# Optimization experiments

Measured on AMD Instinct MI355X. Metric: run time of the kernel, lower is better.

The kernel has to match this reference:

```python
import jax, jax.numpy as jnp
import numpy as np

N = 100000
E = 1600000
EPS = 1e-5


def _layer_norm(x, g, b):
    mu = jnp.mean(x, axis=-1, keepdims=True)
    var = jnp.mean((x - mu) ** 2, axis=-1, keepdims=True)
    return (x - mu) * jax.lax.rsqrt(var + EPS) * g + b


def _sage(x, src, dst, wl, bl, wr):
    # mean aggregation of neighbor messages x[src] into dst, then linear
    msg_sum = jax.ops.segment_sum(x[src], dst, num_segments=N)          # [N, d_in]
    cnt = jax.ops.segment_sum(jnp.ones((src.shape[0],), x.dtype), dst, num_segments=N)
    mean = msg_sum / jnp.maximum(cnt, 1.0)[:, None]
    return mean @ wl.T + bl + x @ wr.T  # lin_l(mean) + lin_r(x), bias only on lin_l


def setup_inputs() -> dict:
    key = jax.random.key(0)
    ks = jax.random.split(key, 16)
    dims = [(9, 64), (64, 128), (128, 128), (128, 128)]
    inp = {
        "x": jax.random.normal(ks[0], (N, 9), dtype=jnp.float32),
        "edge_index": jax.random.randint(ks[1], (2, E), 0, N, dtype=jnp.int32),
    }
    for i, (din, dout) in enumerate(dims, start=1):
        s = 1.0 / np.sqrt(din)
        inp[f"w{i}l"] = jax.random.uniform(ks[2 + 3 * i], (dout, din), jnp.float32, -s, s)
        inp[f"b{i}"] = jnp.zeros((dout,), jnp.float32)
        inp[f"w{i}r"] = jax.random.uniform(ks[3 + 3 * i], (dout, din), jnp.float32, -s, s)
        inp[f"g{i}"] = jnp.ones((dout,), jnp.float32)
        inp[f"be{i}"] = jnp.zeros((dout,), jnp.float32)
    return inp


def reference(x, edge_index,
              w1l, b1, w1r, g1, be1,
              w2l, b2, w2r, g2, be2,
              w3l, b3, w3r, g3, be3,
              w4l, b4, w4r, g4, be4):
    src, dst = edge_index[0], edge_index[1]
    h = jax.nn.relu(_layer_norm(_sage(x, src, dst, w1l, b1, w1r), g1, be1))
    h = jax.nn.relu(_layer_norm(_sage(h, src, dst, w2l, b2, w2r), g2, be2))
    h = jax.nn.relu(_layer_norm(_sage(h, src, dst, w3l, b3, w3r), g3, be3))
    h = _layer_norm(_sage(h, src, dst, w4l, b4, w4r), g4, be4)
    return h
```

## Files before the change

kernel.cpp:

```cpp
#include <hip/hip_runtime.h>
#include <hip/hip_bf16.h>
#include <math.h>

#define N_NODES 100000
#define EPS 1e-5f
#define B2SH 11
#define NPB2 2048
#define NBUCK2 ((N_NODES + NPB2 - 1) / NPB2)
#define NPART 256

typedef __attribute__((ext_vector_type(8))) short bf16x8;
typedef __attribute__((ext_vector_type(4))) float f32x4;

__device__ __forceinline__ float bflo(unsigned int u) { return __uint_as_float(u << 16); }
__device__ __forceinline__ float bfhi(unsigned int u) { return __uint_as_float(u & 0xffff0000u); }
__device__ __forceinline__ unsigned short fbits(float f) {
    __hip_bfloat16 h = __float2bfloat16(f);
    return *reinterpret_cast<unsigned short*>(&h);
}
__device__ __forceinline__ void stv(float* p, float y) { *p = y; }
__device__ __forceinline__ void stv(__hip_bfloat16* p, float y) { *p = __float2bfloat16(y); }
__device__ __forceinline__ unsigned char f8enc(float y) {
    return (unsigned char)((unsigned int)__builtin_amdgcn_cvt_pk_fp8_f32(y, y, 0, false) & 0xffu);
}

__global__ void part_hist(const int* __restrict__ dst, int E, int* __restrict__ blkhist) {
    __shared__ int h[NBUCK2];
    int b = blockIdx.x;
    int slice = (E + NPART - 1) / NPART;
    int s0 = b * slice;
    int s1 = min(E, s0 + slice);
    for (int i = threadIdx.x; i < NBUCK2; i += 256) h[i] = 0;
    __syncthreads();
    for (int e = s0 + threadIdx.x; e < s1; e += 256) atomicAdd(&h[dst[e] >> B2SH], 1);
    __syncthreads();
    for (int i = threadIdx.x; i < NBUCK2; i += 256) blkhist[i * NPART + b] = h[i];
}

__global__ void part_offsets(const int* __restrict__ blkhist, int* __restrict__ blkoffs,
                             int* __restrict__ bbase2, int* __restrict__ row_ptr, int E) {
    __shared__ int tot[NBUCK2];
    __shared__ int sbase[NBUCK2 + 1];
    int j = threadIdx.x;
    if (j < NBUCK2) {
        int run = 0;
#pragma unroll 8
        for (int b = 0; b < NPART; ++b) {
            blkoffs[j * NPART + b] = run;
            run += blkhist[j * NPART + b];
        }
        tot[j] = run;
    }
    __syncthreads();
    if (j == 0) {
        int run = 0;
        for (int i = 0; i < NBUCK2; ++i) {
            sbase[i] = run;
            run += tot[i];
        }
        sbase[NBUCK2] = run;
        row_ptr[N_NODES] = E;
    }
    __syncthreads();
    if (j <= NBUCK2) bbase2[j] = sbase[j];
    if (j < NBUCK2) {
        int base = sbase[j];
#pragma unroll 8
        for (int b = 0; b < NPART; ++b) blkoffs[j * NPART + b] += base;
    }
}

__global__ void part_scatter(const int* __restrict__ src, const int* __restrict__ dst, int E,
                             const int* __restrict__ blkoffs, unsigned int* __restrict__ pairs) {
    __shared__ int pos[NBUCK2];
    int b = blockIdx.x;
    int slice = (E + NPART - 1) / NPART;
    int s0 = b * slice;
    int s1 = min(E, s0 + slice);
    for (int i = threadIdx.x; i < NBUCK2; i += 256) pos[i] = blkoffs[i * NPART + b];
    __syncthreads();
    for (int e = s0 + threadIdx.x; e < s1; e += 256) {
        int d = dst[e];
        int jb = d >> B2SH;
        int p = atomicAdd(&pos[jb], 1);
        pairs[p] = ((unsigned int)src[e] << B2SH) | (unsigned int)(d & (NPB2 - 1));
    }
}

__global__ __launch_bounds__(1024) void bucket_build2(const unsigned int* __restrict__ pairs,
                                                      const int* __restrict__ bbase2,
                                                      int* __restrict__ row_ptr,
                                                      int* __restrict__ col) {
    __shared__ int lcnt[NPB2];
    __shared__ int lofs[NPB2];
    __shared__ int part[1024];
    int bk = blockIdx.x;
    int base = bbase2[bk];
    int cntb = bbase2[bk + 1] - base;
    int node0 = bk << B2SH;
    int t = threadIdx.x;
    lcnt[t] = 0;
    lcnt[t + 1024] = 0;
    __syncthreads();
    for (int i = t; i < cntb; i += 1024) atomicAdd(&lcnt[pairs[base + i] & (NPB2 - 1)], 1);
    __syncthreads();
    int a0 = lcnt[2 * t], a1 = lcnt[2 * t + 1];
    part[t] = a0 + a1;
    __syncthreads();
    for (int off = 1; off < 1024; off <<= 1) {
        int v = (t >= off) ? part[t - off] : 0;
        __syncthreads();
        part[t] += v;
        __syncthreads();
    }
    int excl = part[t] - (a0 + a1);
    lofs[2 * t] = excl;
    lofs[2 * t + 1] = excl + a0;
    __syncthreads();
#pragma unroll
    for (int k = 0; k < 2; ++k) {
        int ln = 2 * t + k;
        int node = node0 + ln;
        if (node < N_NODES) row_ptr[node] = base + lofs[ln];
    }
    lcnt[t] = 0;
    lcnt[t + 1024] = 0;
    __syncthreads();
    for (int i = t; i < cntb; i += 1024) {
        unsigned int v = pairs[base + i];
        int ld = v & (NPB2 - 1);
        int s = v >> B2SH;
        int p = base + lofs[ld] + atomicAdd(&lcnt[ld], 1);
        col[p] = s;
    }
}

__global__ void agg9_kernel(const float* __restrict__ x, const int* __restrict__ row_ptr,
                            const int* __restrict__ col, float* __restrict__ mean, int n) {
    int node = (blockIdx.x * blockDim.x + threadIdx.x) >> 6;
    int lane = threadIdx.x & 63;
    int wv = threadIdx.x >> 6;
    __shared__ float red[4][64];
    float acc = 0.f;
    int start = 0, end = 0;
    if (node < n) {
        start = row_ptr[node];
        end = row_ptr[node + 1];
        int g = lane / 9;
        int f = lane - g * 9;
        if (g < 7 && end > start) {
            for (int p = start + g; p < end; p += 28) {
#pragma unroll
                for (int i = 0; i < 4; ++i) {
                    int q = p + i * 7;
                    int idx = (q < end) ? q : end - 1;
                    float v = x[(size_t)col[idx] * 9 + f];
                    if (q >= end) v = 0.f;
                    acc += v;
                }
            }
        }
    }
    red[wv][lane] = acc;
    __syncthreads();
    if (node < n && lane < 9) {
        float s = red[wv][lane];
#pragma unroll
        for (int k = 1; k < 7; ++k) s += red[wv][lane + 9 * k];
        float inv = 1.f / fmaxf((float)(end - start), 1.f);
        mean[(size_t)node * 9 + lane] = s * inv;
    }
}

__global__ void agg64_kernel(const unsigned char* __restrict__ h8, const int* __restrict__ row_ptr,
                             const int* __restrict__ col, unsigned short* __restrict__ mean, int n) {
    int node = (blockIdx.x * blockDim.x + threadIdx.x) >> 6;
    int lane = threadIdx.x & 63;
    if (node >= n) return;
    int start = row_ptr[node], end = row_ptr[node + 1];
    int deg = end - start;
    if (deg <= 0) {
        mean[(size_t)node * 64 + lane] = 0;
        return;
    }
    const unsigned char* hl = h8 + lane;
    float acc = 0.f;
    int p = start;
    int nfull = start + (deg & ~7);
    for (; p < nfull; p += 8) {
#pragma unroll
        for (int i = 0; i < 8; ++i) {
            unsigned int off = (unsigned int)col[p + i] << 6;
            unsigned int u = (unsigned int)hl[off];
            acc += __builtin_amdgcn_cvt_f32_fp8(u, 0);
        }
    }
    if (p < end) {
#pragma unroll
        for (int i = 0; i < 8; ++i) {
            int q = p + i;
            int idx = (q < end) ? q : p;
            unsigned int off = (unsigned int)col[idx] << 6;
            unsigned int u = (unsigned int)hl[off];
            float v = __builtin_amdgcn_cvt_f32_fp8(u, 0);
            if (q < end) acc += v;
        }
    }
    mean[(size_t)node * 64 + lane] = fbits(acc / (float)deg);
}

__global__ void agg128_kernel(const unsigned char* __restrict__ h8, const int* __restrict__ row_ptr,
                              const int* __restrict__ col, unsigned short* __restrict__ mean, int n) {
    int node = (blockIdx.x * blockDim.x + threadIdx.x) >> 6;
    int lane = threadIdx.x & 63;
    if (node >= n) return;
    int start = row_ptr[node], end = row_ptr[node + 1];
    int deg = end - start;
    if (deg <= 0) {
        *(unsigned int*)&mean[(size_t)node * 128 + lane * 2] = 0u;
        return;
    }
    const unsigned char* hl = h8 + lane * 2;
    float ax = 0.f, ay = 0.f;
    int p = start;
    int nfull = start + (deg & ~7);
    for (; p < nfull; p += 8) {
#pragma unroll
        for (int i = 0; i < 8; ++i) {
            unsigned int off = (unsigned int)col[p + i] << 7;
            unsigned int u = (unsigned int)*(const unsigned short*)(hl + off);
            ax += __builtin_amdgcn_cvt_f32_fp8(u, 0);
            ay += __builtin_amdgcn_cvt_f32_fp8(u, 1);
        }
    }
    if (p < end) {
#pragma unroll
        for (int i = 0; i < 8; ++i) {
            int q = p + i;
            int idx = (q < end) ? q : p;
            unsigned int off = (unsigned int)col[idx] << 7;
            unsigned int u = (unsigned int)*(const unsigned short*)(hl + off);
            float v0 = __builtin_amdgcn_cvt_f32_fp8(u, 0);
            float v1 = __builtin_amdgcn_cvt_f32_fp8(u, 1);
            if (q < end) {
                ax += v0;
                ay += v1;
            }
        }
    }
    float inv = 1.f / (float)deg;
    unsigned int lo = fbits(ax * inv);
    unsigned int hi = fbits(ay * inv);
    *(unsigned int*)&mean[(size_t)node * 128 + lane * 2] = lo | (hi << 16);
}

__global__ void wtrans_kernel(const float* __restrict__ wl, const float* __restrict__ wr,
                              int din, int dout, float* __restrict__ wt) {
    int i = blockIdx.x * blockDim.x + threadIdx.x;
    int K2 = 2 * din;
    if (i >= K2 * dout) return;
    int k = i / dout, j = i % dout;
    wt[k * dout + j] = (k < din) ? wl[j * din + k] : wr[j * din + (k - din)];
}

__global__ void packw_kernel(const float* __restrict__ wl, const float* __restrict__ wr,
                             int din, unsigned short* __restrict__ bpack) {
    int K2 = 2 * din;
    int total = K2 * 128;
    int i = blockIdx.x * 256 + threadIdx.x;
    if (i >= total) return;
    int e = i & 7;
    int lane = (i >> 3) & 63;
    int rest = i >> 9;
    int KSTEPS = din / 16;
    int t = rest / KSTEPS, ks = rest % KSTEPS;
    int j = t * 16 + (lane & 15);
    int k = ks * 32 + (lane >> 4) * 8 + e;
    float w = (k < din) ? wl[j * din + k] : wr[j * din + (k - din)];
    bpack[i] = fbits(w);
}

template <int DIN, int DOUT, bool RELU, typename OT>
__global__ __launch_bounds__(256) void linear_ln_kernel(
    const float* __restrict__ meanp, const float* __restrict__ hp,
    const float* __restrict__ wt, const float* __restrict__ bias,
    const float* __restrict__ g, const float* __restrict__ be,
    OT* __restrict__ out, unsigned char* __restrict__ out8, int n) {
    constexpr int K2 = 2 * DIN;
    constexpr int NCOL = DOUT / 4;
    constexpr int NROW = 256 / NCOL;
    constexpr int TN = 4 * NROW;
    constexpr int ASTR = TN + 4;
    constexpr int OSTR = DOUT + 4;
    constexpr int SMEMF = (K2 * ASTR > TN * OSTR) ? K2 * ASTR : TN * OSTR;
    __shared__ float smem[SMEMF];

    int tid = threadIdx.x;
    int n0base = blockIdx.x * TN;

    for (int idx = tid; idx < TN * K2; idx += 256) {
        int nn = idx / K2;
        int k = idx % K2;
        int node = n0base + nn;
        float v = 0.f;
        if (node < n)
            v = (k < DIN) ? meanp[(size_t)node * DIN + k] : hp[(size_t)node * DIN + (k - DIN)];
        smem[k * ASTR + nn] = v;
    }
    __syncthreads();

    int colt = tid % NCOL;
    int rowt = tid / NCOL;
    int j0 = colt * 4;
    int nn0 = rowt * 4;

    float acc[4][4];
#pragma unroll
    for (int i = 0; i < 4; ++i)
#pragma unroll
        for (int j = 0; j < 4; ++j) acc[i][j] = 0.f;

#pragma unroll 2
    for (int k = 0; k < K2; ++k) {
        float4 a = *(const float4*)&smem[k * ASTR + nn0];
        float4 w = *(const float4*)&wt[k * DOUT + j0];
        acc[0][0] = fmaf(a.x, w.x, acc[0][0]);
        acc[0][1] = fmaf(a.x, w.y, acc[0][1]);
        acc[0][2] = fmaf(a.x, w.z, acc[0][2]);
        acc[0][3] = fmaf(a.x, w.w, acc[0][3]);
        acc[1][0] = fmaf(a.y, w.x, acc[1][0]);
        acc[1][1] = fmaf(a.y, w.y, acc[1][1]);
        acc[1][2] = fmaf(a.y, w.z, acc[1][2]);
        acc[1][3] = fmaf(a.y, w.w, acc[1][3]);
        acc[2][0] = fmaf(a.z, w.x, acc[2][0]);
        acc[2][1] = fmaf(a.z, w.y, acc[2][1]);
        acc[2][2] = fmaf(a.z, w.z, acc[2][2]);
        acc[2][3] = fmaf(a.z, w.w, acc[2][3]);
        acc[3][0] = fmaf(a.w, w.x, acc[3][0]);
        acc[3][1] = fmaf(a.w, w.y, acc[3][1]);
        acc[3][2] = fmaf(a.w, w.z, acc[3][2]);
        acc[3][3] = fmaf(a.w, w.w, acc[3][3]);
    }
    __syncthreads();

    float4 bj = *(const float4*)&bias[j0];
#pragma unroll
    for (int i = 0; i < 4; ++i) {
        float4 o;
        o.x = acc[i][0] + bj.x;
        o.y = acc[i][1] + bj.y;
        o.z = acc[i][2] + bj.z;
        o.w = acc[i][3] + bj.w;
        *(float4*)&smem[(nn0 + i) * OSTR + j0] = o;
    }
    __syncthreads();

    int wid = tid >> 6, lane = tid & 63;
    for (int nn = wid; nn < TN; nn += 4) {
        int node = n0base + nn;
        if (node >= n) continue;
        float v0 = smem[nn * OSTR + lane];
        float v1 = (DOUT == 128) ? smem[nn * OSTR + 64 + lane] : 0.f;
        float s = v0 + v1;
        float ss = v0 * v0 + v1 * v1;
#pragma unroll
        for (int off = 32; off > 0; off >>= 1) {
            s += __shfl_xor(s, off);
            ss += __shfl_xor(ss, off);
        }
        float mu = s / DOUT;
        float var = ss / DOUT - mu * mu;
        float inv = rsqrtf(var + EPS);
        float y0 = (v0 - mu) * inv * g[lane] + be[lane];
        if (RELU) y0 = fmaxf(y0, 0.f);
        stv(&out[(size_t)node * DOUT + lane], y0);
        if (out8) out8[(size_t)node * DOUT + lane] = f8enc(y0);
        if (DOUT == 128) {
            float y1 = (v1 - mu) * inv * g[64 + lane] + be[64 + lane];
            if (RELU) y1 = fmaxf(y1, 0.f);
            stv(&out[(size_t)node * DOUT + 64 + lane], y1);
            if (out8) out8[(size_t)node * DOUT + 64 + lane] = f8enc(y1);
        }
    }
}

template <int DIN, bool RELU, typename OT>
__global__ __launch_bounds__(256) void mfma_linear_ln(
    const unsigned short* __restrict__ meanb, const unsigned short* __restrict__ hb,
    const unsigned short* __restrict__ bpack, const float* __restrict__ bias,
    const float* __restrict__ g, const float* __restrict__ be, OT* __restrict__ out,
    unsigned char* __restrict__ out8, int n) {
    constexpr int KSTEPS = DIN / 16;
    int tid = threadIdx.x;
    int w = tid >> 6, l = tid & 63;
    int n0 = blockIdx.x * 64 + w * 16;
    int arow = l & 15;
    int koff = (l >> 4) * 8;
    int anode = n0 + arow;
    if (anode >= n) anode = n - 1;
    const unsigned short* mrow = meanb + (size_t)anode * DIN;
    const unsigned short* hrow = hb + (size_t)anode * DIN;

    f32x4 acc[8];
#pragma unroll
    for (int t = 0; t < 8; ++t) acc[t] = (f32x4){0.f, 0.f, 0.f, 0.f};

#pragma unroll
    for (int ks = 0; ks < KSTEPS; ++ks) {
        int k = ks * 32 + koff;
        const unsigned short* ap = (k < DIN) ? (mrow + k) : (hrow + (k - DIN));
        bf16x8 a = *(const bf16x8*)ap;
#pragma unroll
        for (int t = 0; t < 8; ++t) {
            bf16x8 b = *(const bf16x8*)(bpack + (((size_t)t * KSTEPS + ks) * 64 + l) * 8);
            acc[t] = __builtin_amdgcn_mfma_f32_16x16x32_bf16(a, b, acc[t], 0, 0, 0);
        }
    }

    int jbase = l & 15;
    float bj[8], gj[8], bej[8];
#pragma unroll
    for (int t = 0; t < 8; ++t) {
        bj[t] = bias[t * 16 + jbase];
        gj[t] = g[t * 16 + jbase];
        bej[t] = be[t * 16 + jbase];
    }
#pragma unroll
    for (int r = 0; r < 4; ++r) {
        float v[8];
        float s = 0.f, ss = 0.f;
#pragma unroll
        for (int t = 0; t < 8; ++t) {
            v[t] = acc[t][r] + bj[t];
            s += v[t];
            ss += v[t] * v[t];
        }
#pragma unroll
        for (int off = 1; off < 16; off <<= 1) {
            s += __shfl_xor(s, off);
            ss += __shfl_xor(ss, off);
        }
        float mu = s * (1.f / 128.f);
        float var = ss * (1.f / 128.f) - mu * mu;
        float inv = rsqrtf(var + EPS);
        int node = n0 + (l >> 4) * 4 + r;
        if (node < n) {
#pragma unroll
            for (int t = 0; t < 8; ++t) {
                float y = (v[t] - mu) * inv * gj[t] + bej[t];
                if (RELU) y = fmaxf(y, 0.f);
                stv(&out[(size_t)node * 128 + t * 16 + jbase], y);
                if (out8) out8[(size_t)node * 128 + t * 16 + jbase] = f8enc(y);
            }
        }
    }
}

extern "C" void kernel_launch(void* const* d_in, const int* in_sizes, int n_in,
                              void* d_out, int out_size, void* d_ws, size_t ws_size,
                              hipStream_t stream) {
    const float* x = (const float*)d_in[0];
    const int* edge = (const int*)d_in[1];
    int E = in_sizes[1] / 2;
    const int* src = edge;
    const int* dst = edge + E;

    const float* w1l = (const float*)d_in[2];
    const float* b1  = (const float*)d_in[3];
    const float* w1r = (const float*)d_in[4];
    const float* g1  = (const float*)d_in[5];
    const float* be1 = (const float*)d_in[6];
    const float* w2l = (const float*)d_in[7];
    const float* b2  = (const float*)d_in[8];
    const float* w2r = (const float*)d_in[9];
    const float* g2  = (const float*)d_in[10];
    const float* be2 = (const float*)d_in[11];
    const float* w3l = (const float*)d_in[12];
    const float* b3  = (const float*)d_in[13];
    const float* w3r = (const float*)d_in[14];
    const float* g3  = (const float*)d_in[15];
    const float* be3 = (const float*)d_in[16];
    const float* w4l = (const float*)d_in[17];
    const float* b4  = (const float*)d_in[18];
    const float* w4r = (const float*)d_in[19];
    const float* g4  = (const float*)d_in[20];
    const float* be4 = (const float*)d_in[21];

    char* ws = (char*)d_ws;
    size_t off = 0;
    auto alloc = [&](size_t bytes) {
        void* p = ws + off;
        off = (off + bytes + 255) & ~(size_t)255;
        return p;
    };
    int* row_ptr = (int*)alloc((N_NODES + 1) * sizeof(int));
    int* blkhist = (int*)alloc((size_t)NBUCK2 * NPART * sizeof(int));
    int* blkoffs = (int*)alloc((size_t)NBUCK2 * NPART * sizeof(int));
    int* bbase2  = (int*)alloc((NBUCK2 + 1) * sizeof(int));
    unsigned int* pairs = (unsigned int*)alloc((size_t)E * sizeof(unsigned int));
    int* colx    = (int*)alloc((size_t)E * sizeof(int));
    float* wt1   = (float*)alloc(18 * 64 * sizeof(float));
    unsigned short* bp2 = (unsigned short*)alloc(128 * 128 * sizeof(short));
    unsigned short* bp3 = (unsigned short*)alloc(256 * 128 * sizeof(short));
    unsigned short* bp4 = (unsigned short*)alloc(256 * 128 * sizeof(short));
    float* m9    = (float*)alloc((size_t)N_NODES * 9 * sizeof(float));
    unsigned short* mbf = (unsigned short*)alloc((size_t)N_NODES * 128 * sizeof(short));
    unsigned short* h1  = (unsigned short*)alloc((size_t)N_NODES * 64 * sizeof(short));
    unsigned short* h2  = (unsigned short*)alloc((size_t)N_NODES * 128 * sizeof(short));
    unsigned short* h3  = (unsigned short*)alloc((size_t)N_NODES * 128 * sizeof(short));
    unsigned char* h1f8 = (unsigned char*)alloc((size_t)N_NODES * 64);
    unsigned char* h2f8 = (unsigned char*)alloc((size_t)N_NODES * 128);
    unsigned char* h3f8 = (unsigned char*)alloc((size_t)N_NODES * 128);
    (void)ws_size;

    part_hist<<<NPART, 256, 0, stream>>>(dst, E, blkhist);
    part_offsets<<<1, 64, 0, stream>>>(blkhist, blkoffs, bbase2, row_ptr, E);
    part_scatter<<<NPART, 256, 0, stream>>>(src, dst, E, blkoffs, pairs);
    bucket_build2<<<NBUCK2, 1024, 0, stream>>>(pairs, bbase2, row_ptr, colx);

    wtrans_kernel<<<(18 * 64 + 255) / 256, 256, 0, stream>>>(w1l, w1r, 9, 64, wt1);
    packw_kernel<<<(128 * 128 + 255) / 256, 256, 0, stream>>>(w2l, w2r, 64, bp2);
    packw_kernel<<<(256 * 128 + 255) / 256, 256, 0, stream>>>(w3l, w3r, 128, bp3);
    packw_kernel<<<(256 * 128 + 255) / 256, 256, 0, stream>>>(w4l, w4r, 128, bp4);

    float* out = (float*)d_out;
    int AGB = (N_NODES * 64 + 255) / 256;
    int LNB = (N_NODES + 63) / 64;

    agg9_kernel<<<AGB, 256, 0, stream>>>(x, row_ptr, colx, m9, N_NODES);
    linear_ln_kernel<9, 64, true, __hip_bfloat16><<<LNB, 256, 0, stream>>>(
        m9, x, wt1, b1, g1, be1, (__hip_bfloat16*)h1, h1f8, N_NODES);
    agg64_kernel<<<AGB, 256, 0, stream>>>(h1f8, row_ptr, colx, mbf, N_NODES);
    mfma_linear_ln<64, true, __hip_bfloat16><<<LNB, 256, 0, stream>>>(
        mbf, h1, bp2, b2, g2, be2, (__hip_bfloat16*)h2, h2f8, N_NODES);
    agg128_kernel<<<AGB, 256, 0, stream>>>(h2f8, row_ptr, colx, mbf, N_NODES);
    mfma_linear_ln<128, true, __hip_bfloat16><<<LNB, 256, 0, stream>>>(
        mbf, h2, bp3, b3, g3, be3, (__hip_bfloat16*)h3, h3f8, N_NODES);
    agg128_kernel<<<AGB, 256, 0, stream>>>(h3f8, row_ptr, colx, mbf, N_NODES);
    mfma_linear_ln<128, false, float><<<LNB, 256, 0, stream>>>(
        mbf, h3, bp4, b4, g4, be4, out, (unsigned char*)nullptr, N_NODES);
}
```

Measured before the change: 404.5 us.

## Gather fp8 neighbor rows with 16-byte loads across multiple edges per wavefront

The 64- and 128-wide aggregation kernels now give each lane a 16-byte chunk of a neighbor row, so one wavefront processes 16 edges per iteration instead of one edge with 1-2 byte loads per lane. Partial sums are combined with cross-lane xor shuffles and written back as packed bf16 with 16-byte stores. This cuts the number of memory instructions and raises the number of independent gathers in flight. In exchange it adds shuffle-reduction overhead and wastes lanes on low-degree nodes (average degree is about 16).

```diff
diff --git a/kernel.cpp b/kernel.cpp
--- a/kernel.cpp
+++ b/kernel.cpp
@@ -13,7 +13,6 @@
 typedef __attribute__((ext_vector_type(4))) float f32x4;
 
 __device__ __forceinline__ float bflo(unsigned int u) { return __uint_as_float(u << 16); }
-__device__ __forceinline__ float bfhi(unsigned int u) { return __uint_as_float(u & 0xffff0000u); }
 __device__ __forceinline__ unsigned short fbits(float f) {
     __hip_bfloat16 h = __float2bfloat16(f);
     return *reinterpret_cast<unsigned short*>(&h);
@@ -172,41 +171,56 @@
     }
 }
 
+__device__ __forceinline__ void acc16_fp8(const uint4& v, float* acc) {
+#pragma unroll
+    for (int d = 0; d < 4; ++d) {
+        unsigned int u = (&v.x)[d];
+        acc[d * 4 + 0] += __builtin_amdgcn_cvt_f32_fp8(u, 0);
+        acc[d * 4 + 1] += __builtin_amdgcn_cvt_f32_fp8(u, 1);
+        acc[d * 4 + 2] += __builtin_amdgcn_cvt_f32_fp8(u, 2);
+        acc[d * 4 + 3] += __builtin_amdgcn_cvt_f32_fp8(u, 3);
+    }
+}
+
 __global__ void agg64_kernel(const unsigned char* __restrict__ h8, const int* __restrict__ row_ptr,
                              const int* __restrict__ col, unsigned short* __restrict__ mean, int n) {
     int node = (blockIdx.x * blockDim.x + threadIdx.x) >> 6;
     int lane = threadIdx.x & 63;
     if (node >= n) return;
+    int e = lane >> 2, c = lane & 3;
     int start = row_ptr[node], end = row_ptr[node + 1];
     int deg = end - start;
-    if (deg <= 0) {
-        mean[(size_t)node * 64 + lane] = 0;
-        return;
-    }
-    const unsigned char* hl = h8 + lane;
-    float acc = 0.f;
-    int p = start;
-    int nfull = start + (deg & ~7);
-    for (; p < nfull; p += 8) {
-#pragma unroll
-        for (int i = 0; i < 8; ++i) {
-            unsigned int off = (unsigned int)col[p + i] << 6;
-            unsigned int u = (unsigned int)hl[off];
-            acc += __builtin_amdgcn_cvt_f32_fp8(u, 0);
-        }
-    }
-    if (p < end) {
-#pragma unroll
-        for (int i = 0; i < 8; ++i) {
-            int q = p + i;
-            int idx = (q < end) ? q : p;
-            unsigned int off = (unsigned int)col[idx] << 6;
-            unsigned int u = (unsigned int)hl[off];
-            float v = __builtin_amdgcn_cvt_f32_fp8(u, 0);
-            if (q < end) acc += v;
-        }
-    }
-    mean[(size_t)node * 64 + lane] = fbits(acc / (float)deg);
+    float acc[16];
+#pragma unroll
+    for (int j = 0; j < 16; ++j) acc[j] = 0.f;
+    const unsigned char* hc = h8 + c * 16;
+    for (int p = start; p < end; p += 16) {
+        int q = p + e;
+        int idx = col[(q < end) ? q : end - 1];
+        uint4 v = *(const uint4*)(hc + ((size_t)idx << 6));
+        if (q >= end) v = (uint4){0u, 0u, 0u, 0u};
+        acc16_fp8(v, acc);
+    }
+#pragma unroll
+    for (int j = 0; j < 16; ++j) {
+        acc[j] += __shfl_xor(acc[j], 4);
+        acc[j] += __shfl_xor(acc[j], 8);
+        acc[j] += __shfl_xor(acc[j], 16);
+        acc[j] += __shfl_xor(acc[j], 32);
+    }
+    if (e == 0) {
+        float inv = 1.f / fmaxf((float)deg, 1.f);
+        unsigned int w[8];
+#pragma unroll
+        for (int j = 0; j < 8; ++j) {
+            unsigned int lo = fbits(acc[2 * j] * inv);
+            unsigned int hi = fbits(acc[2 * j + 1] * inv);
+            w[j] = lo | (hi << 16);
+        }
+        unsigned short* mrow = mean + (size_t)node * 64 + c * 16;
+        *(uint4*)(mrow) = (uint4){w[0], w[1], w[2], w[3]};
+        *(uint4*)(mrow + 8) = (uint4){w[4], w[5], w[6], w[7]};
+    }
 }
 
 __global__ void agg128_kernel(const unsigned char* __restrict__ h8, const int* __restrict__ row_ptr,
@@ -214,44 +228,44 @@
     int node = (blockIdx.x * blockDim.x + threadIdx.x) >> 6;
     int lane = threadIdx.x & 63;
     if (node >= n) return;
+    int e = lane >> 3, c = lane & 7;
     int start = row_ptr[node], end = row_ptr[node + 1];
     int deg = end - start;
-    if (deg <= 0) {
-        *(unsigned int*)&mean[(size_t)node * 128 + lane * 2] = 0u;
-        return;
-    }
-    const unsigned char* hl = h8 + lane * 2;
-    float ax = 0.f, ay = 0.f;
-    int p = start;
-    int nfull = start + (deg & ~7);
-    for (; p < nfull; p += 8) {
-#pragma unroll
-        for (int i = 0; i < 8; ++i) {
-            unsigned int off = (unsigned int)col[p + i] << 7;
-            unsigned int u = (unsigned int)*(const unsigned short*)(hl + off);
-            ax += __builtin_amdgcn_cvt_f32_fp8(u, 0);
-            ay += __builtin_amdgcn_cvt_f32_fp8(u, 1);
-        }
-    }
-    if (p < end) {
-#pragma unroll
-        for (int i = 0; i < 8; ++i) {
-            int q = p + i;
-            int idx = (q < end) ? q : p;
-            unsigned int off = (unsigned int)col[idx] << 7;
-            unsigned int u = (unsigned int)*(const unsigned short*)(hl + off);
-            float v0 = __builtin_amdgcn_cvt_f32_fp8(u, 0);
-            float v1 = __builtin_amdgcn_cvt_f32_fp8(u, 1);
-            if (q < end) {
-                ax += v0;
-                ay += v1;
-            }
-        }
-    }
-    float inv = 1.f / (float)deg;
-    unsigned int lo = fbits(ax * inv);
-    unsigned int hi = fbits(ay * inv);
-    *(unsigned int*)&mean[(size_t)node * 128 + lane * 2] = lo | (hi << 16);
+    float acc[16];
+#pragma unroll
+    for (int j = 0; j < 16; ++j) acc[j] = 0.f;
+    const unsigned char* hc = h8 + c * 16;
+    for (int p = start; p < end; p += 16) {
+        int qa = p + e;
+        int qb = p + 8 + e;
+        int ia = col[(qa < end) ? qa : end - 1];
+        int ib = col[(qb < end) ? qb : end - 1];
+        uint4 va = *(const uint4*)(hc + ((size_t)ia << 7));
+        uint4 vb = *(const uint4*)(hc + ((size_t)ib << 7));
+        if (qa >= end) va = (uint4){0u, 0u, 0u, 0u};
+        if (qb >= end) vb = (uint4){0u, 0u, 0u, 0u};
+        acc16_fp8(va, acc);
+        acc16_fp8(vb, acc);
+    }
+#pragma unroll
+    for (int j = 0; j < 16; ++j) {
+        acc[j] += __shfl_xor(acc[j], 8);
+        acc[j] += __shfl_xor(acc[j], 16);
+        acc[j] += __shfl_xor(acc[j], 32);
+    }
+    if (e == 0) {
+        float inv = 1.f / fmaxf((float)deg, 1.f);
+        unsigned int w[8];
+#pragma unroll
+        for (int j = 0; j < 8; ++j) {
+            unsigned int lo = fbits(acc[2 * j] * inv);
+            unsigned int hi = fbits(acc[2 * j + 1] * inv);
+            w[j] = lo | (hi << 16);
+        }
+        unsigned short* mrow = mean + (size_t)node * 128 + c * 16;
+        *(uint4*)(mrow) = (uint4){w[0], w[1], w[2], w[3]};
+        *(uint4*)(mrow + 8) = (uint4){w[4], w[5], w[6], w[7]};
+    }
 }
 
 __global__ void wtrans_kernel(const float* __restrict__ wl, const float* __restrict__ wr,
```

Result: faster. 389.7 us (-3.7%).
